# Kernel tuning notes

Measured on AMD Instinct MI355X. Metric: run time of the kernel, lower is better.

## Reference

```python
import jax, jax.numpy as jnp
import numpy as np

C = 17
BETA = 0.95
ALPHA = 5.0
WPC = 3.0  # weight_per_class
IGNORE = 255


def setup_inputs() -> dict:
    key = jax.random.key(0)
    k1, k2 = jax.random.split(key)
    pred = jax.random.normal(k1, (2, C, 200, 200, 16), dtype=jnp.float32)
    ssc_target = jax.random.randint(k2, (2, 200, 200, 16), 0, C, dtype=jnp.int64)
    f1_list = jnp.zeros((C,), dtype=jnp.float32)  # running F1 buffer
    return {"pred": pred, "ssc_target": ssc_target, "f1_list": f1_list}


def _bce_ones(x):
    # F.binary_cross_entropy(x, ones) = -log(x), with torch's log clamp at -100
    return jnp.minimum(-jnp.log(jnp.maximum(x, 1e-38)), 100.0)


def _sem_scal_loss(pred, ssc_target, f1_list):
    B = pred.shape[0]
    ps = jax.nn.softmax(pred, axis=1)                      # [B,C,X,Y,Z]
    mask = (ssc_target != IGNORE)                          # [B,X,Y,Z]
    mf = mask.astype(ps.dtype)
    tgt = jnp.where(mask, ssc_target, 0)                   # safe class index

    # prob of the target class at each voxel -> per-class nominator via segment_sum
    p_at = jnp.take_along_axis(ps, tgt[:, None], axis=1)[:, 0]          # [B,X,Y,Z]
    tgt_flat = tgt.reshape(-1)
    mflat = mf.reshape(-1)
    nominator = jax.ops.segment_sum(p_at.reshape(-1) * mflat, tgt_flat, num_segments=C)
    sum_comp = jax.ops.segment_sum(mflat, tgt_flat, num_segments=C)     # |{target==i}| in mask
    sum_p = jnp.einsum('bcn,bn->c', ps.reshape(B, C, -1), mf.reshape(B, -1))
    n_mask = jnp.sum(mflat)

    has = sum_comp > 0
    precision = jnp.where(sum_p > 0, nominator / jnp.where(sum_p > 0, sum_p, 1.0), 0.0)
    recall = jnp.where(has, nominator / jnp.where(has, sum_comp, 1.0), 0.0)
    neg_comp = n_mask - sum_comp                           # sum(1 - completion_target)
    spec_num = (n_mask - sum_p) - (sum_comp - nominator)   # sum((1-p)*(1-comp))
    specificity = jnp.where(neg_comp > 0, spec_num / jnp.where(neg_comp > 0, neg_comp, 1.0), 0.0)

    loss_list = jnp.where(
        has,
        jnp.where(sum_p > 0, _bce_ones(precision), 0.0)
        + _bce_ones(recall)
        + jnp.where(neg_comp > 0, _bce_ones(specificity), 0.0),
        0.0,
    )

    denom = precision + recall
    f1 = jnp.where(denom > 0, 2.0 * precision * recall / jnp.where(denom > 0, denom, 1.0), 0.0)
    cur_f1 = jnp.where(has, f1, 0.0)
    new_f1 = BETA * f1_list + (1.0 - BETA) * cur_f1        # updated running buffer

    count = jnp.sum(has.astype(ps.dtype))
    weight_pool = WPC * count

    sel = loss_list != 0
    logits = jnp.where(sel, ALPHA * (1.0 - new_f1), -jnp.inf)
    sm = jax.nn.softmax(logits)                            # softmax over selected classes
    weighted = loss_list * (1.0 + weight_pool * sm)
    loss = jnp.sum(weighted) / (count * (1.0 + WPC))
    return loss


def reference(pred, ssc_target, f1_list):
    return _sem_scal_loss(pred, ssc_target, f1_list)
```

## Files before the change

### kernel.cpp

```cpp
#include <hip/hip_runtime.h>
#include <math.h>

#define NC 17
#define PLANE 640000
#define H2 (PLANE / 2)
#define BPB1 1250
#define NBLK1 (2 * BPB1)
#define PCOLS 2504
#define BETA_C 0.95f
#define ALPHA_C 5.0f
#define WPC_C 3.0f
#define IGNORE_C 255

#define DPP_ADD(v, ctrl)                                                        \
    do {                                                                        \
        int _t = __builtin_amdgcn_update_dpp(0, __float_as_int(v), (ctrl),      \
                                             0xf, 0xf, true);                   \
        (v) += __int_as_float(_t);                                              \
    } while (0)

__device__ __forceinline__ float wave_sum_dpp(float v) {
    DPP_ADD(v, 0x111);
    DPP_ADD(v, 0x112);
    DPP_ADD(v, 0x114);
    DPP_ADD(v, 0x118);
    DPP_ADD(v, 0x142);
    DPP_ADD(v, 0x143);
    return v;
}


__global__ __launch_bounds__(256) void al_reduce1(const float* __restrict__ pred,
                                                  const int* __restrict__ tgt,
                                                  float* __restrict__ part) {
    const int bb = blockIdx.x;
    const int b  = (bb >= BPB1) ? 1 : 0;
    const int n2 = (bb - b * BPB1) * 256 + (int)threadIdx.x;
    const float2* p0 = reinterpret_cast<const float2*>(pred)
                       + (size_t)(b * NC) * H2 + n2;
    const int2 t2 = reinterpret_cast<const int2*>(tgt)[b * H2 + n2];

    float2 x[NC];
#pragma unroll
    for (int c = 0; c < NC; ++c) x[c] = p0[(size_t)c * H2];

    float2 s = make_float2(0.f, 0.f);
#pragma unroll
    for (int c = 0; c < NC; ++c) {
        x[c].x = __expf(x[c].x); s.x += x[c].x;
        x[c].y = __expf(x[c].y); s.y += x[c].y;
    }

    const float i0 = (t2.x != IGNORE_C) ? __builtin_amdgcn_rcpf(s.x) : 0.0f;
    const float i1 = (t2.y != IGNORE_C) ? __builtin_amdgcn_rcpf(s.y) : 0.0f;

    __shared__ float lds[3 * NC];
    if (threadIdx.x < 3 * NC) lds[threadIdx.x] = 0.f;
    __syncthreads();

    float et0 = 0.f, et1 = 0.f;
    float sump[NC];
#pragma unroll
    for (int c = 0; c < NC; ++c) {
        sump[c] = x[c].x * i0 + x[c].y * i1;
        et0 = (c == t2.x) ? x[c].x : et0;
        et1 = (c == t2.y) ? x[c].y : et1;
    }

    if (t2.x != IGNORE_C) { atomicAdd(&lds[t2.x], et0 * i0); atomicAdd(&lds[2 * NC + t2.x], 1.0f); }
    if (t2.y != IGNORE_C) { atomicAdd(&lds[t2.y], et1 * i1); atomicAdd(&lds[2 * NC + t2.y], 1.0f); }

#pragma unroll
    for (int c = 0; c < NC; ++c) sump[c] = wave_sum_dpp(sump[c]);
    if ((threadIdx.x & 63) == 63) {
#pragma unroll
        for (int c = 0; c < NC; ++c) atomicAdd(&lds[NC + c], sump[c]);
    }
    __syncthreads();

    if (threadIdx.x < 3 * NC)
        part[(size_t)threadIdx.x * PCOLS + bb] = lds[threadIdx.x];
}

__global__ __launch_bounds__(256) void al_reduce2(const float* __restrict__ part,
                                                  float* __restrict__ acc) {
    const int r = blockIdx.x;
    const int tid = (int)threadIdx.x;
    const float4* p = reinterpret_cast<const float4*>(part + (size_t)r * PCOLS);

    float s = 0.f;
#pragma unroll
    for (int k = 0; k < 3; ++k) {
        const int i = tid + k * 256;
        if (i < 625) {
            const float4 v = p[i];
            s += (v.x + v.y) + (v.z + v.w);
        }
    }
    s = wave_sum_dpp(s);

    __shared__ float w[4];
    if ((tid & 63) == 63) w[tid >> 6] = s;
    __syncthreads();
    if (tid == 0) acc[r] = (w[0] + w[1]) + (w[2] + w[3]);
}

__device__ __forceinline__ float bce_ones(float x) {
    return fminf(-logf(fmaxf(x, 1e-38f)), 100.0f);
}

__global__ void al_finalize(const float* __restrict__ acc,
                            const float* __restrict__ f1_list,
                            float* __restrict__ out) {
    if (threadIdx.x != 0 || blockIdx.x != 0) return;

    float nom[NC], sump[NC], cnt[NC];
    float n_mask = 0.f;
    for (int c = 0; c < NC; ++c) {
        nom[c]  = acc[c];
        sump[c] = acc[NC + c];
        cnt[c]  = acc[2 * NC + c];
        n_mask += cnt[c];
    }

    float loss_list[NC], newf1[NC];
    float count = 0.f;
    for (int c = 0; c < NC; ++c) {
        const bool has = cnt[c] > 0.f;
        const float prec = (sump[c] > 0.f) ? nom[c] / sump[c] : 0.f;
        const float rec  = has ? nom[c] / cnt[c] : 0.f;
        const float negc = n_mask - cnt[c];
        const float spec_num = (n_mask - sump[c]) - (cnt[c] - nom[c]);
        const float spec = (negc > 0.f) ? spec_num / negc : 0.f;

        float ll = 0.f;
        if (has) {
            ll  = (sump[c] > 0.f) ? bce_ones(prec) : 0.f;
            ll += bce_ones(rec);
            ll += (negc > 0.f) ? bce_ones(spec) : 0.f;
        }
        loss_list[c] = ll;

        const float den = prec + rec;
        const float f1  = (den > 0.f) ? 2.f * prec * rec / den : 0.f;
        const float cur = has ? f1 : 0.f;
        newf1[c] = BETA_C * f1_list[c] + (1.f - BETA_C) * cur;
        count += has ? 1.f : 0.f;
    }

    const float wp = WPC_C * count;

    float mxl = -INFINITY;
    for (int c = 0; c < NC; ++c) {
        const float lg = (loss_list[c] != 0.f) ? ALPHA_C * (1.f - newf1[c]) : -INFINITY;
        mxl = fmaxf(mxl, lg);
    }
    float e[NC];
    float se = 0.f;
    for (int c = 0; c < NC; ++c) {
        const float lg = (loss_list[c] != 0.f) ? ALPHA_C * (1.f - newf1[c]) : -INFINITY;
        e[c] = expf(lg - mxl);
        se += e[c];
    }

    float total = 0.f;
    for (int c = 0; c < NC; ++c) {
        const float sm = e[c] / se;
        total += loss_list[c] * (1.f + wp * sm);
    }
    out[0] = total / (count * (1.f + WPC_C));
}

extern "C" void kernel_launch(void* const* d_in, const int* in_sizes, int n_in,
                              void* d_out, int out_size, void* d_ws, size_t ws_size,
                              hipStream_t stream) {
    const float* pred    = (const float*)d_in[0];
    const int*   tgt     = (const int*)d_in[1];
    const float* f1_list = (const float*)d_in[2];
    float* out  = (float*)d_out;
    float* part = (float*)d_ws;
    float* acc  = part + (size_t)(3 * NC) * PCOLS;

    al_reduce1<<<dim3(NBLK1), dim3(256), 0, stream>>>(pred, tgt, part);
    al_reduce2<<<dim3(3 * NC), dim3(256), 0, stream>>>(part, acc);
    al_finalize<<<dim3(1), dim3(64), 0, stream>>>(acc, f1_list, out);
}
```

Measured before the change: 37.83 us.

## Process five slabs per block with double-buffered register loads

```diff
diff --git a/kernel.cpp b/kernel.cpp
--- a/kernel.cpp
+++ b/kernel.cpp
@@ -4,9 +4,10 @@
 #define NC 17
 #define PLANE 640000
 #define H2 (PLANE / 2)
-#define BPB1 1250
-#define NBLK1 (2 * BPB1)
-#define PCOLS 2504
+#define J 5
+#define BPB 250
+#define NBLK1 (2 * BPB)
+#define PCOLS 504
 #define BETA_C 0.95f
 #define ALPHA_C 5.0f
 #define WPC_C 3.0f
@@ -33,69 +34,93 @@
 __global__ __launch_bounds__(256) void al_reduce1(const float* __restrict__ pred,
                                                   const int* __restrict__ tgt,
                                                   float* __restrict__ part) {
-    const int bb = blockIdx.x;
-    const int b  = (bb >= BPB1) ? 1 : 0;
-    const int n2 = (bb - b * BPB1) * 256 + (int)threadIdx.x;
-    const float2* p0 = reinterpret_cast<const float2*>(pred)
-                       + (size_t)(b * NC) * H2 + n2;
-    const int2 t2 = reinterpret_cast<const int2*>(tgt)[b * H2 + n2];
-
-    float2 x[NC];
-#pragma unroll
-    for (int c = 0; c < NC; ++c) x[c] = p0[(size_t)c * H2];
-
-    float2 s = make_float2(0.f, 0.f);
-#pragma unroll
-    for (int c = 0; c < NC; ++c) {
-        x[c].x = __expf(x[c].x); s.x += x[c].x;
-        x[c].y = __expf(x[c].y); s.y += x[c].y;
-    }
-
-    const float i0 = (t2.x != IGNORE_C) ? __builtin_amdgcn_rcpf(s.x) : 0.0f;
-    const float i1 = (t2.y != IGNORE_C) ? __builtin_amdgcn_rcpf(s.y) : 0.0f;
+    const int bb  = blockIdx.x;
+    const int b   = (bb >= BPB) ? 1 : 0;
+    const int base = (bb - b * BPB) * (256 * J);
+    const int tid = (int)threadIdx.x;
+    const float2* p0 = reinterpret_cast<const float2*>(pred) + (size_t)(b * NC) * H2;
+    const int2*   tg = reinterpret_cast<const int2*>(tgt) + (size_t)b * H2;
 
     __shared__ float lds[3 * NC];
-    if (threadIdx.x < 3 * NC) lds[threadIdx.x] = 0.f;
+    if (tid < 3 * NC) lds[tid] = 0.f;
+
+    float sump[NC];
+#pragma unroll
+    for (int c = 0; c < NC; ++c) sump[c] = 0.f;
+
+    float2 xA[NC], xB[NC];
+    int2 tA, tB;
+
+#define LOAD_SLAB(X, T, s)                                                      \
+    do {                                                                        \
+        const int n2 = base + (s) * 256 + tid;                                  \
+        _Pragma("unroll")                                                       \
+        for (int c = 0; c < NC; ++c) X[c] = p0[(size_t)c * H2 + n2];            \
+        T = tg[n2];                                                             \
+    } while (0)
+
+#define COMP_SLAB(X, T)                                                         \
+    do {                                                                        \
+        float2 ss = make_float2(0.f, 0.f);                                      \
+        _Pragma("unroll")                                                       \
+        for (int c = 0; c < NC; ++c) {                                          \
+            X[c].x = __expf(X[c].x); ss.x += X[c].x;                            \
+            X[c].y = __expf(X[c].y); ss.y += X[c].y;                            \
+        }                                                                       \
+        const float j0 = (T.x != IGNORE_C) ? __builtin_amdgcn_rcpf(ss.x) : 0.f; \
+        const float j1 = (T.y != IGNORE_C) ? __builtin_amdgcn_rcpf(ss.y) : 0.f; \
+        float e0 = 0.f, e1 = 0.f;                                               \
+        _Pragma("unroll")                                                       \
+        for (int c = 0; c < NC; ++c) {                                          \
+            sump[c] += X[c].x * j0 + X[c].y * j1;                               \
+            e0 = (c == T.x) ? X[c].x : e0;                                      \
+            e1 = (c == T.y) ? X[c].y : e1;                                      \
+        }                                                                       \
+        if (T.x != IGNORE_C) { atomicAdd(&lds[T.x], e0 * j0);                   \
+                               atomicAdd(&lds[2 * NC + T.x], 1.0f); }           \
+        if (T.y != IGNORE_C) { atomicAdd(&lds[T.y], e1 * j1);                   \
+                               atomicAdd(&lds[2 * NC + T.y], 1.0f); }           \
+    } while (0)
+
+    LOAD_SLAB(xA, tA, 0);
+    LOAD_SLAB(xB, tB, 1);
     __syncthreads();
 
-    float et0 = 0.f, et1 = 0.f;
-    float sump[NC];
-#pragma unroll
-    for (int c = 0; c < NC; ++c) {
-        sump[c] = x[c].x * i0 + x[c].y * i1;
-        et0 = (c == t2.x) ? x[c].x : et0;
-        et1 = (c == t2.y) ? x[c].y : et1;
-    }
-
-    if (t2.x != IGNORE_C) { atomicAdd(&lds[t2.x], et0 * i0); atomicAdd(&lds[2 * NC + t2.x], 1.0f); }
-    if (t2.y != IGNORE_C) { atomicAdd(&lds[t2.y], et1 * i1); atomicAdd(&lds[2 * NC + t2.y], 1.0f); }
+    COMP_SLAB(xA, tA);
+    LOAD_SLAB(xA, tA, 2);
+    COMP_SLAB(xB, tB);
+    LOAD_SLAB(xB, tB, 3);
+    COMP_SLAB(xA, tA);
+    LOAD_SLAB(xA, tA, 4);
+    COMP_SLAB(xB, tB);
+    COMP_SLAB(xA, tA);
+
+#undef LOAD_SLAB
+#undef COMP_SLAB
 
 #pragma unroll
     for (int c = 0; c < NC; ++c) sump[c] = wave_sum_dpp(sump[c]);
-    if ((threadIdx.x & 63) == 63) {
+    if ((tid & 63) == 63) {
 #pragma unroll
         for (int c = 0; c < NC; ++c) atomicAdd(&lds[NC + c], sump[c]);
     }
     __syncthreads();
 
-    if (threadIdx.x < 3 * NC)
-        part[(size_t)threadIdx.x * PCOLS + bb] = lds[threadIdx.x];
+    if (tid < 3 * NC)
+        part[(size_t)tid * PCOLS + bb] = lds[tid];
 }
 
 __global__ __launch_bounds__(256) void al_reduce2(const float* __restrict__ part,
                                                   float* __restrict__ acc) {
     const int r = blockIdx.x;
     const int tid = (int)threadIdx.x;
-    const float4* p = reinterpret_cast<const float4*>(part + (size_t)r * PCOLS);
+    const float* p = part + (size_t)r * PCOLS;
 
     float s = 0.f;
 #pragma unroll
-    for (int k = 0; k < 3; ++k) {
+    for (int k = 0; k < 2; ++k) {
         const int i = tid + k * 256;
-        if (i < 625) {
-            const float4 v = p[i];
-            s += (v.x + v.y) + (v.z + v.w);
-        }
+        s += (i < NBLK1) ? p[i] : 0.f;
     }
     s = wave_sum_dpp(s);
 
```

New measurement: 36.01 us. 1.05x faster.
